# Optimization experiments

Hardware: AMD Instinct MI355X
Metric: run time of the kernel (lower is better)

Reference implementation:

```python
import jax, jax.numpy as jnp
import numpy as np

BETA = 0.45
GAMMA = 0.45
EPS = 1e-12  # F.normalize eps

N_PRED = 16384
N_GT = 32768


def setup_inputs() -> dict:
    key = jax.random.key(0)
    k1, k2, k3, k4 = jax.random.split(key, 4)
    pred_feat = jax.random.normal(k1, (N_PRED, 6), dtype=jnp.float32)
    gt_data = jax.random.normal(k2, (N_GT, 6), dtype=jnp.float32)
    R = jax.random.normal(k3, (3, 3), dtype=jnp.float32)
    t = jax.random.normal(k4, (3,), dtype=jnp.float32)
    s = jnp.ones((1,), dtype=jnp.float32)
    return {"pred_feat": pred_feat, "gt_data": gt_data, "R": R, "t": t, "s": s}


def _l2_normalize(x):
    # matches F.normalize(p=2, dim=1, eps=1e-12): x / max(||x||, eps)
    n = jnp.linalg.norm(x, axis=-1, keepdims=True)
    return x / jnp.maximum(n, EPS)


def reference(pred_feat, gt_data, R, t, s):
    # --- registration loss (R,t,s come from the external TEASER++ solver) ---
    I = jnp.eye(3, dtype=R.dtype)
    rot_loss = jnp.linalg.norm(R - I)          # Frobenius norm
    trans_loss = jnp.linalg.norm(t)            # L2 norm
    scale_loss = (s[0] - 1.0) ** 2
    reg_loss = rot_loss + trans_loss + scale_loss

    # --- nearest-neighbor normal loss ---
    pred_points = pred_feat[:, :3]   # [N,3]
    pred_normals = pred_feat[:, 3:]  # [N,3]
    gt_points = gt_data[:, :3]       # [L,3]
    gt_normals = gt_data[:, 3:]      # [L,3]

    # squared euclidean distances [N,L]; argmin identical to cdist argmin
    p2 = jnp.sum(pred_points * pred_points, axis=1, keepdims=True)  # [N,1]
    g2 = jnp.sum(gt_points * gt_points, axis=1)                     # [L]
    d2 = p2 + g2[None, :] - 2.0 * (pred_points @ gt_points.T)       # [N,L]
    min_indices = jnp.argmin(d2, axis=1)                            # [N]

    closest_gt_normals = gt_normals[min_indices]                    # [N,3]
    pred_u = _l2_normalize(pred_normals)
    gt_u = _l2_normalize(closest_gt_normals)
    cos_theta = jnp.sum(pred_u * gt_u, axis=1)
    norm_loss = jnp.mean(1.0 - cos_theta)

    return BETA * reg_loss + GAMMA * norm_loss
```

## Files before the change

kernel.cpp:

```cpp
#include <hip/hip_runtime.h>
#include <math.h>

#define NPRED 16384
#define NGT   32768
#define BETA  0.45f
#define GAMMA 0.45f

#define NGROUP 16
#define SPG    4
#define GSPLIT (NGROUP * SPG)
#define NTILE  (NGT / 32)
#define TPS    (NTILE / GSPLIT)
#define PB     256
#define NN_BX  (NPRED / PB)
#define RESB   (NPRED / 8)

typedef float f32x16 __attribute__((ext_vector_type(16)));
typedef short short8 __attribute__((ext_vector_type(8)));

__device__ __forceinline__ unsigned bf16h(float f) {
    unsigned u = __float_as_uint(f);
    return (u + 0x7FFFu + ((u >> 16) & 1u)) >> 16;
}
__device__ __forceinline__ float bf16f(unsigned h) { return __uint_as_float(h << 16); }
__device__ __forceinline__ unsigned pk2(unsigned lo, unsigned hi) { return lo | (hi << 16); }

#define MFMA_V(D, A, B, ZC)                                                    \
    asm("v_mfma_f32_32x32x16_bf16 %0, %1, %2, %3"                              \
        : "=&v"(D) : "v"(A), "v"(B), "v"(ZC))

__device__ __forceinline__ float tile_key(const f32x16 acc, int gtile) {
    const float m0 = fminf(fminf(acc[0],  acc[1]),  acc[2]);
    const float m1 = fminf(fminf(acc[3],  acc[4]),  acc[5]);
    const float m2 = fminf(fminf(acc[6],  acc[7]),  acc[8]);
    const float m3 = fminf(fminf(acc[9],  acc[10]), acc[11]);
    const float m4 = fminf(fminf(acc[12], acc[13]), acc[14]);
    const float n0 = fminf(fminf(m0, m1), m2);
    const float n1 = fminf(fminf(m3, m4), acc[15]);
    const float tmin = fminf(n0, n1);
    return __uint_as_float((__float_as_uint(tmin) & 0xFFFFFC00u) | (unsigned)gtile);
}

__global__ __launch_bounds__(256) void nn_kernel(
    const float* __restrict__ pred,
    const float* __restrict__ gt,
    unsigned* __restrict__ packed2)
{
    __shared__ uint4 AF[TPS * 64];

    const int l  = threadIdx.x & 63;
    const int w  = threadIdx.x >> 6;

    const int pbase = blockIdx.x * PB + w * 64;
    const int c     = l & 31;
    const bool hi   = l >= 32;
    uint4 bu0, bu1;
    {
        const int pi = pbase + c;
        const float x = pred[pi * 6 + 0], y = pred[pi * 6 + 1], zc = pred[pi * 6 + 2];
        const float mx = -2.0f * x, my = -2.0f * y, mz = -2.0f * zc;
        const unsigned xh = bf16h(mx), yh = bf16h(my), zh = bf16h(mz);
        const unsigned xl = bf16h(mx - bf16f(xh)), yl = bf16h(my - bf16f(yh));
        const unsigned zl = bf16h(mz - bf16f(zh));
        bu0.x = hi ? pk2(zh, zl) : pk2(xh, xl);
        bu0.y = bu0.x;
        bu0.z = hi ? 0x3F803F80u : pk2(yh, yl);
        bu0.w = hi ? 0u : bu0.z;
    }
    {
        const int pi = pbase + 32 + c;
        const float x = pred[pi * 6 + 0], y = pred[pi * 6 + 1], zc = pred[pi * 6 + 2];
        const float mx = -2.0f * x, my = -2.0f * y, mz = -2.0f * zc;
        const unsigned xh = bf16h(mx), yh = bf16h(my), zh = bf16h(mz);
        const unsigned xl = bf16h(mx - bf16f(xh)), yl = bf16h(my - bf16f(yh));
        const unsigned zl = bf16h(mz - bf16f(zh));
        bu1.x = hi ? pk2(zh, zl) : pk2(xh, xl);
        bu1.y = bu1.x;
        bu1.z = hi ? 0x3F803F80u : pk2(yh, yl);
        bu1.w = hi ? 0u : bu1.z;
    }
    const short8 bv0 = *(const short8*)&bu0;
    const short8 bv1 = *(const short8*)&bu1;
    const f32x16 zacc = {0.f,0.f,0.f,0.f,0.f,0.f,0.f,0.f,
                         0.f,0.f,0.f,0.f,0.f,0.f,0.f,0.f};

    float kmin0 = 1e30f, kmin1 = 1e30f;

#pragma unroll 1
    for (int u = 0; u < SPG; ++u) {
        const int sp = blockIdx.y * SPG + u;

        __syncthreads();
#pragma unroll
        for (int k = 0; k < 2; ++k) {
            const int lrow = threadIdx.x + k * 256;
            const int j = sp * (TPS * 32) + lrow;
            const float x = gt[j * 6 + 0], y = gt[j * 6 + 1], z = gt[j * 6 + 2];
            const float g2 = fmaf(x, x, fmaf(y, y, z * z));
            const unsigned xh = bf16h(x),  yh = bf16h(y),  zh = bf16h(z),  gh = bf16h(g2);
            const unsigned xl = bf16h(x - bf16f(xh)), yl = bf16h(y - bf16f(yh));
            const unsigned zl = bf16h(z - bf16f(zh)), gl = bf16h(g2 - bf16f(gh));
            const int tl = lrow >> 5, r = lrow & 31;
            AF[tl * 64 + r]      = make_uint4(pk2(xh, xh), pk2(xl, xl), pk2(yh, yh), pk2(yl, yl));
            AF[tl * 64 + 32 + r] = make_uint4(pk2(zh, zh), pk2(zl, zl), pk2(gh, gl), 0u);
        }
        __syncthreads();

        const int t0 = sp * TPS;
#pragma unroll 2
        for (int tt = 0; tt < TPS; tt += 2) {
            const uint4 aua = AF[tt * 64 + l];
            const uint4 aub = AF[(tt + 1) * 64 + l];
            const short8 ava = *(const short8*)&aua;
            const short8 avb = *(const short8*)&aub;
            const int ga = t0 + tt, gb = t0 + tt + 1;

            f32x16 acc_a0, acc_b0, acc_a1, acc_b1;
            MFMA_V(acc_a0, ava, bv0, zacc);
            MFMA_V(acc_b0, avb, bv0, zacc);
            MFMA_V(acc_a1, ava, bv1, zacc);
            MFMA_V(acc_b1, avb, bv1, zacc);

            kmin0 = fminf(kmin0, fminf(tile_key(acc_a0, ga), tile_key(acc_b0, gb)));
            kmin1 = fminf(kmin1, fminf(tile_key(acc_a1, ga), tile_key(acc_b1, gb)));
        }
    }

    kmin0 = fminf(kmin0, __shfl_xor(kmin0, 32, 64));
    kmin1 = fminf(kmin1, __shfl_xor(kmin1, 32, 64));

    const float km = hi ? kmin1 : kmin0;
    packed2[(size_t)(pbase + l) * NGROUP + blockIdx.y] = __float_as_uint(km);
}

__global__ __launch_bounds__(256) void rescan_kernel(
    const float* __restrict__ pred,
    const float* __restrict__ gt,
    const unsigned* __restrict__ packed2,
    float* __restrict__ partials)
{
    __shared__ float part[8];
    const int w = threadIdx.x >> 6, l = threadIdx.x & 63;
    const int half = l >> 5, jl = l & 31;
    const int pi = blockIdx.x * 8 + w * 2 + half;

    const unsigned* kp = packed2 + (size_t)pi * NGROUP;
    float e = (jl < NGROUP) ? __uint_as_float(kp[jl]) : 1e30f;
#pragma unroll
    for (int off = 16; off; off >>= 1)
        e = fminf(e, __shfl_xor(e, off, 32));
    const unsigned tix = __float_as_uint(e) & 0x3FFu;

    const int row = (int)tix * 32 + jl;
    const float2* gr = (const float2*)(gt + row * 6);
    const float2 ga = gr[0], gb = gr[1];
    const float gx = ga.x, gy = ga.y, gz = gb.x;
    const float g2 = fmaf(gx, gx, fmaf(gy, gy, gz * gz));
    const float2* pr = (const float2*)(pred + pi * 6);
    const float2 pa = pr[0], pb = pr[1];
    const float px = pa.x, py = pa.y, pz = pb.x;
    float d = fmaf(px, -2.0f * gx, fmaf(py, -2.0f * gy, fmaf(pz, -2.0f * gz, g2)));
    int jj = jl;
#pragma unroll
    for (int off = 16; off; off >>= 1) {
        const float d2 = __shfl_xor(d, off, 32);
        const int   j2 = __shfl_xor(jj, off, 32);
        const bool t = (d2 < d) || (d2 == d && j2 < jj);
        d  = t ? d2 : d;
        jj = t ? j2 : jj;
    }
    if (jl == 0) {
        const int idx = (int)tix * 32 + jj;
        const float nx = pred[pi * 6 + 3], ny = pred[pi * 6 + 4], nz = pred[pi * 6 + 5];
        const float ax = gt[idx * 6 + 3],  ay = gt[idx * 6 + 4],  az = gt[idx * 6 + 5];
        const float pn = fmaxf(sqrtf(fmaf(nx, nx, fmaf(ny, ny, nz * nz))), 1e-12f);
        const float gn = fmaxf(sqrtf(fmaf(ax, ax, fmaf(ay, ay, az * az))), 1e-12f);
        part[w * 2 + half] = 1.0f - fmaf(nx, ax, fmaf(ny, ay, nz * az)) / (pn * gn);
    }
    __syncthreads();
    if (threadIdx.x == 0) {
        float s = 0.f;
#pragma unroll
        for (int i = 0; i < 8; ++i) s += part[i];
        partials[blockIdx.x] = s;
    }
}

__global__ __launch_bounds__(256) void final_kernel(
    const float* __restrict__ partials,
    const float* __restrict__ Rm,
    const float* __restrict__ tv,
    const float* __restrict__ sv,
    float* __restrict__ out)
{
    __shared__ float ws_[4];
    float s = 0.f;
    for (int i = threadIdx.x; i < RESB; i += 256) s += partials[i];
#pragma unroll
    for (int off = 32; off; off >>= 1) s += __shfl_down(s, off, 64);
    if ((threadIdx.x & 63) == 0) ws_[threadIdx.x >> 6] = s;
    __syncthreads();
    if (threadIdx.x == 0) {
        const float t = ws_[0] + ws_[1] + ws_[2] + ws_[3];
        float rs = 0.f;
#pragma unroll
        for (int k = 0; k < 9; ++k) {
            const float v = Rm[k] - ((k % 4 == 0) ? 1.0f : 0.0f);
            rs = fmaf(v, v, rs);
        }
        const float rot = sqrtf(rs);
        const float tr  = sqrtf(fmaf(tv[0], tv[0], fmaf(tv[1], tv[1], tv[2] * tv[2])));
        const float sc  = (sv[0] - 1.0f) * (sv[0] - 1.0f);
        out[0] = GAMMA * t / (float)NPRED + BETA * (rot + tr + sc);
    }
}

extern "C" void kernel_launch(void* const* d_in, const int* in_sizes, int n_in,
                              void* d_out, int out_size, void* d_ws, size_t ws_size,
                              hipStream_t stream)
{
    const float* pred = (const float*)d_in[0];
    const float* gt   = (const float*)d_in[1];
    const float* Rm   = (const float*)d_in[2];
    const float* tv   = (const float*)d_in[3];
    const float* sv   = (const float*)d_in[4];
    float* out = (float*)d_out;

    unsigned* packed2 = (unsigned*)d_ws;
    float* partials   = (float*)((char*)d_ws + (size_t)NPRED * NGROUP * 4);

    nn_kernel<<<dim3(NN_BX, NGROUP), 256, 0, stream>>>(pred, gt, packed2);
    rescan_kernel<<<RESB, 256, 0, stream>>>(pred, gt, packed2, partials);
    final_kernel<<<1, 256, 0, stream>>>(partials, Rm, tv, sv, out);
}
```

Baseline: 34.81 us.

## Double-buffer GT tiles in LDS and hand-code min3 reductions via inline asm

Loads of the next GT chunk from global memory are issued before the MFMA loop over the current chunk, and are converted into a second LDS buffer afterwards. This hides global-load latency and cuts the barriers per chunk from two to one. The per-tile min reduction and key packing are rewritten with inline v_min3_f32 and v_and_or_b32, giving fewer VALU instructions per tile. The cost is double the LDS footprint and the loses of compiler scheduling freedom around the inline asm.

```diff
diff --git a/kernel.cpp b/kernel.cpp
--- a/kernel.cpp
+++ b/kernel.cpp
@@ -29,16 +29,29 @@
     asm("v_mfma_f32_32x32x16_bf16 %0, %1, %2, %3"                              \
         : "=&v"(D) : "v"(A), "v"(B), "v"(ZC))
 
-__device__ __forceinline__ float tile_key(const f32x16 acc, int gtile) {
-    const float m0 = fminf(fminf(acc[0],  acc[1]),  acc[2]);
-    const float m1 = fminf(fminf(acc[3],  acc[4]),  acc[5]);
-    const float m2 = fminf(fminf(acc[6],  acc[7]),  acc[8]);
-    const float m3 = fminf(fminf(acc[9],  acc[10]), acc[11]);
-    const float m4 = fminf(fminf(acc[12], acc[13]), acc[14]);
-    const float n0 = fminf(fminf(m0, m1), m2);
-    const float n1 = fminf(fminf(m3, m4), acc[15]);
-    const float tmin = fminf(n0, n1);
-    return __uint_as_float((__float_as_uint(tmin) & 0xFFFFFC00u) | (unsigned)gtile);
+__device__ __forceinline__ float tile_key3(const f32x16 acc, float vmask, int gtile) {
+    float m0, m1, m2, m3, m4, n0, n1, key;
+    asm("v_min3_f32 %0, %1, %2, %3" : "=v"(m0) : "v"(acc[0]),  "v"(acc[1]),  "v"(acc[2]));
+    asm("v_min3_f32 %0, %1, %2, %3" : "=v"(m1) : "v"(acc[3]),  "v"(acc[4]),  "v"(acc[5]));
+    asm("v_min3_f32 %0, %1, %2, %3" : "=v"(m2) : "v"(acc[6]),  "v"(acc[7]),  "v"(acc[8]));
+    asm("v_min3_f32 %0, %1, %2, %3" : "=v"(m3) : "v"(acc[9]),  "v"(acc[10]), "v"(acc[11]));
+    asm("v_min3_f32 %0, %1, %2, %3" : "=v"(m4) : "v"(acc[12]), "v"(acc[13]), "v"(acc[14]));
+    asm("v_min3_f32 %0, %1, %2, %3" : "=v"(n0) : "v"(m0), "v"(m1), "v"(m2));
+    asm("v_min3_f32 %0, %1, %2, %3" : "=v"(n1) : "v"(m3), "v"(m4), "v"(acc[15]));
+    asm("v_min_f32 %0, %1, %2"      : "=v"(key) : "v"(n0), "v"(n1));
+    asm("v_and_or_b32 %0, %1, %2, %3" : "+v"(key) : "v"(vmask), "s"(gtile));
+    return key;
+}
+
+__device__ __forceinline__ void conv_row(float x, float y, float z,
+                                         uint4* __restrict__ buf, int lrow) {
+    const float g2 = fmaf(x, x, fmaf(y, y, z * z));
+    const unsigned xh = bf16h(x),  yh = bf16h(y),  zh = bf16h(z),  gh = bf16h(g2);
+    const unsigned xl = bf16h(x - bf16f(xh)), yl = bf16h(y - bf16f(yh));
+    const unsigned zl = bf16h(z - bf16f(zh)), gl = bf16h(g2 - bf16f(gh));
+    const int tl = lrow >> 5, r = lrow & 31;
+    buf[tl * 64 + r]      = make_uint4(pk2(xh, xh), pk2(xl, xl), pk2(yh, yh), pk2(yl, yl));
+    buf[tl * 64 + 32 + r] = make_uint4(pk2(zh, zh), pk2(zl, zl), pk2(gh, gl), 0u);
 }
 
 __global__ __launch_bounds__(256) void nn_kernel(
@@ -46,7 +59,7 @@
     const float* __restrict__ gt,
     unsigned* __restrict__ packed2)
 {
-    __shared__ uint4 AF[TPS * 64];
+    __shared__ uint4 AF[2][TPS * 64];
 
     const int l  = threadIdx.x & 63;
     const int w  = threadIdx.x >> 6;
@@ -83,34 +96,43 @@
     const short8 bv1 = *(const short8*)&bu1;
     const f32x16 zacc = {0.f,0.f,0.f,0.f,0.f,0.f,0.f,0.f,
                          0.f,0.f,0.f,0.f,0.f,0.f,0.f,0.f};
+    const float vmask = __uint_as_float(0xFFFFFC00u);
 
     float kmin0 = 1e30f, kmin1 = 1e30f;
+    const int sp0 = blockIdx.y * SPG;
+
+    float2 r0a, r0b, r1a, r1b;
+    {
+        const int j0 = sp0 * 512 + threadIdx.x;
+        const float2* p0 = (const float2*)(gt + j0 * 6);
+        const float2* p1 = (const float2*)(gt + (j0 + 256) * 6);
+        r0a = p0[0]; r0b = p0[1];
+        r1a = p1[0]; r1b = p1[1];
+    }
+    conv_row(r0a.x, r0a.y, r0b.x, AF[0], threadIdx.x);
+    conv_row(r1a.x, r1a.y, r1b.x, AF[0], threadIdx.x + 256);
+    __syncthreads();
 
 #pragma unroll 1
     for (int u = 0; u < SPG; ++u) {
-        const int sp = blockIdx.y * SPG + u;
-
-        __syncthreads();
-#pragma unroll
-        for (int k = 0; k < 2; ++k) {
-            const int lrow = threadIdx.x + k * 256;
-            const int j = sp * (TPS * 32) + lrow;
-            const float x = gt[j * 6 + 0], y = gt[j * 6 + 1], z = gt[j * 6 + 2];
-            const float g2 = fmaf(x, x, fmaf(y, y, z * z));
-            const unsigned xh = bf16h(x),  yh = bf16h(y),  zh = bf16h(z),  gh = bf16h(g2);
-            const unsigned xl = bf16h(x - bf16f(xh)), yl = bf16h(y - bf16f(yh));
-            const unsigned zl = bf16h(z - bf16f(zh)), gl = bf16h(g2 - bf16f(gh));
-            const int tl = lrow >> 5, r = lrow & 31;
-            AF[tl * 64 + r]      = make_uint4(pk2(xh, xh), pk2(xl, xl), pk2(yh, yh), pk2(yl, yl));
-            AF[tl * 64 + 32 + r] = make_uint4(pk2(zh, zh), pk2(zl, zl), pk2(gh, gl), 0u);
-        }
-        __syncthreads();
+        const int sp = sp0 + u;
+        uint4* cur = AF[u & 1];
+        uint4* nxt = AF[(u + 1) & 1];
+        const bool more = (u + 1 < SPG);
+
+        if (more) {
+            const int j0 = (sp + 1) * 512 + threadIdx.x;
+            const float2* p0 = (const float2*)(gt + j0 * 6);
+            const float2* p1 = (const float2*)(gt + (j0 + 256) * 6);
+            r0a = p0[0]; r0b = p0[1];
+            r1a = p1[0]; r1b = p1[1];
+        }
 
         const int t0 = sp * TPS;
 #pragma unroll 2
         for (int tt = 0; tt < TPS; tt += 2) {
-            const uint4 aua = AF[tt * 64 + l];
-            const uint4 aub = AF[(tt + 1) * 64 + l];
+            const uint4 aua = cur[tt * 64 + l];
+            const uint4 aub = cur[(tt + 1) * 64 + l];
             const short8 ava = *(const short8*)&aua;
             const short8 avb = *(const short8*)&aub;
             const int ga = t0 + tt, gb = t0 + tt + 1;
@@ -121,9 +143,19 @@
             MFMA_V(acc_a1, ava, bv1, zacc);
             MFMA_V(acc_b1, avb, bv1, zacc);
 
-            kmin0 = fminf(kmin0, fminf(tile_key(acc_a0, ga), tile_key(acc_b0, gb)));
-            kmin1 = fminf(kmin1, fminf(tile_key(acc_a1, ga), tile_key(acc_b1, gb)));
-        }
+            const float ka0 = tile_key3(acc_a0, vmask, ga);
+            const float kb0 = tile_key3(acc_b0, vmask, gb);
+            asm("v_min3_f32 %0, %0, %1, %2" : "+v"(kmin0) : "v"(ka0), "v"(kb0));
+            const float ka1 = tile_key3(acc_a1, vmask, ga);
+            const float kb1 = tile_key3(acc_b1, vmask, gb);
+            asm("v_min3_f32 %0, %0, %1, %2" : "+v"(kmin1) : "v"(ka1), "v"(kb1));
+        }
+
+        if (more) {
+            conv_row(r0a.x, r0a.y, r0b.x, nxt, threadIdx.x);
+            conv_row(r1a.x, r1a.y, r1b.x, nxt, threadIdx.x + 256);
+        }
+        __syncthreads();
     }
 
     kmin0 = fminf(kmin0, __shfl_xor(kmin0, 32, 64));
```

Result: faster. 31.41 us (-9.8%).

## Split GT across 64 grid blocks, use min3 asm reductions and setprio

Applied to the files above, without the earlier changes.

Removes the per-block loop over four GT sub-tiles, so each block now stages one 512-point GT tile and the grid grows from 16 to 64 splits in y. This drops the repeated syncthreads and staging stalls and adds parallelism. The tile-min reduction is rewritten in inline asm using v_min3_f32 and v_and_or_b32 to cut VALU instruction count, and s_setprio is raised around the MFMA loop. The cost is four times more packed partial keys written and read by the rescan kernel.

```diff
diff --git a/kernel.cpp b/kernel.cpp
--- a/kernel.cpp
+++ b/kernel.cpp
@@ -6,9 +6,7 @@
 #define BETA  0.45f
 #define GAMMA 0.45f
 
-#define NGROUP 16
-#define SPG    4
-#define GSPLIT (NGROUP * SPG)
+#define GSPLIT 64
 #define NTILE  (NGT / 32)
 #define TPS    (NTILE / GSPLIT)
 #define PB     256
@@ -29,16 +27,18 @@
     asm("v_mfma_f32_32x32x16_bf16 %0, %1, %2, %3"                              \
         : "=&v"(D) : "v"(A), "v"(B), "v"(ZC))
 
-__device__ __forceinline__ float tile_key(const f32x16 acc, int gtile) {
-    const float m0 = fminf(fminf(acc[0],  acc[1]),  acc[2]);
-    const float m1 = fminf(fminf(acc[3],  acc[4]),  acc[5]);
-    const float m2 = fminf(fminf(acc[6],  acc[7]),  acc[8]);
-    const float m3 = fminf(fminf(acc[9],  acc[10]), acc[11]);
-    const float m4 = fminf(fminf(acc[12], acc[13]), acc[14]);
-    const float n0 = fminf(fminf(m0, m1), m2);
-    const float n1 = fminf(fminf(m3, m4), acc[15]);
-    const float tmin = fminf(n0, n1);
-    return __uint_as_float((__float_as_uint(tmin) & 0xFFFFFC00u) | (unsigned)gtile);
+__device__ __forceinline__ float tile_key3(const f32x16 acc, float vmask, int gtile) {
+    float m0, m1, m2, m3, m4, n0, n1, key;
+    asm("v_min3_f32 %0, %1, %2, %3" : "=v"(m0) : "v"(acc[0]),  "v"(acc[1]),  "v"(acc[2]));
+    asm("v_min3_f32 %0, %1, %2, %3" : "=v"(m1) : "v"(acc[3]),  "v"(acc[4]),  "v"(acc[5]));
+    asm("v_min3_f32 %0, %1, %2, %3" : "=v"(m2) : "v"(acc[6]),  "v"(acc[7]),  "v"(acc[8]));
+    asm("v_min3_f32 %0, %1, %2, %3" : "=v"(m3) : "v"(acc[9]),  "v"(acc[10]), "v"(acc[11]));
+    asm("v_min3_f32 %0, %1, %2, %3" : "=v"(m4) : "v"(acc[12]), "v"(acc[13]), "v"(acc[14]));
+    asm("v_min3_f32 %0, %1, %2, %3" : "=v"(n0) : "v"(m0), "v"(m1), "v"(m2));
+    asm("v_min3_f32 %0, %1, %2, %3" : "=v"(n1) : "v"(m3), "v"(m4), "v"(acc[15]));
+    asm("v_min_f32 %0, %1, %2"      : "=v"(key) : "v"(n0), "v"(n1));
+    asm("v_and_or_b32 %0, %1, %2, %3" : "+v"(key) : "v"(vmask), "s"(gtile));
+    return key;
 }
 
 __global__ __launch_bounds__(256) void nn_kernel(
@@ -50,6 +50,21 @@
 
     const int l  = threadIdx.x & 63;
     const int w  = threadIdx.x >> 6;
+    const int sp = blockIdx.y;
+
+#pragma unroll
+    for (int k = 0; k < 2; ++k) {
+        const int lrow = threadIdx.x + k * 256;
+        const int j = sp * 512 + lrow;
+        const float x = gt[j * 6 + 0], y = gt[j * 6 + 1], z = gt[j * 6 + 2];
+        const float g2 = fmaf(x, x, fmaf(y, y, z * z));
+        const unsigned xh = bf16h(x),  yh = bf16h(y),  zh = bf16h(z),  gh = bf16h(g2);
+        const unsigned xl = bf16h(x - bf16f(xh)), yl = bf16h(y - bf16f(yh));
+        const unsigned zl = bf16h(z - bf16f(zh)), gl = bf16h(g2 - bf16f(gh));
+        const int tl = lrow >> 5, r = lrow & 31;
+        AF[tl * 64 + r]      = make_uint4(pk2(xh, xh), pk2(xl, xl), pk2(yh, yh), pk2(yl, yl));
+        AF[tl * 64 + 32 + r] = make_uint4(pk2(zh, zh), pk2(zl, zl), pk2(gh, gl), 0u);
+    }
 
     const int pbase = blockIdx.x * PB + w * 64;
     const int c     = l & 31;
@@ -83,54 +98,41 @@
     const short8 bv1 = *(const short8*)&bu1;
     const f32x16 zacc = {0.f,0.f,0.f,0.f,0.f,0.f,0.f,0.f,
                          0.f,0.f,0.f,0.f,0.f,0.f,0.f,0.f};
+    const float vmask = __uint_as_float(0xFFFFFC00u);
 
     float kmin0 = 1e30f, kmin1 = 1e30f;
-
-#pragma unroll 1
-    for (int u = 0; u < SPG; ++u) {
-        const int sp = blockIdx.y * SPG + u;
-
-        __syncthreads();
-#pragma unroll
-        for (int k = 0; k < 2; ++k) {
-            const int lrow = threadIdx.x + k * 256;
-            const int j = sp * (TPS * 32) + lrow;
-            const float x = gt[j * 6 + 0], y = gt[j * 6 + 1], z = gt[j * 6 + 2];
-            const float g2 = fmaf(x, x, fmaf(y, y, z * z));
-            const unsigned xh = bf16h(x),  yh = bf16h(y),  zh = bf16h(z),  gh = bf16h(g2);
-            const unsigned xl = bf16h(x - bf16f(xh)), yl = bf16h(y - bf16f(yh));
-            const unsigned zl = bf16h(z - bf16f(zh)), gl = bf16h(g2 - bf16f(gh));
-            const int tl = lrow >> 5, r = lrow & 31;
-            AF[tl * 64 + r]      = make_uint4(pk2(xh, xh), pk2(xl, xl), pk2(yh, yh), pk2(yl, yl));
-            AF[tl * 64 + 32 + r] = make_uint4(pk2(zh, zh), pk2(zl, zl), pk2(gh, gl), 0u);
-        }
-        __syncthreads();
-
-        const int t0 = sp * TPS;
+    __syncthreads();
+
+    __builtin_amdgcn_s_setprio(1);
+    const int t0 = sp * TPS;
 #pragma unroll 2
-        for (int tt = 0; tt < TPS; tt += 2) {
-            const uint4 aua = AF[tt * 64 + l];
-            const uint4 aub = AF[(tt + 1) * 64 + l];
-            const short8 ava = *(const short8*)&aua;
-            const short8 avb = *(const short8*)&aub;
-            const int ga = t0 + tt, gb = t0 + tt + 1;
-
-            f32x16 acc_a0, acc_b0, acc_a1, acc_b1;
-            MFMA_V(acc_a0, ava, bv0, zacc);
-            MFMA_V(acc_b0, avb, bv0, zacc);
-            MFMA_V(acc_a1, ava, bv1, zacc);
-            MFMA_V(acc_b1, avb, bv1, zacc);
-
-            kmin0 = fminf(kmin0, fminf(tile_key(acc_a0, ga), tile_key(acc_b0, gb)));
-            kmin1 = fminf(kmin1, fminf(tile_key(acc_a1, ga), tile_key(acc_b1, gb)));
-        }
-    }
+    for (int tt = 0; tt < TPS; tt += 2) {
+        const uint4 aua = AF[tt * 64 + l];
+        const uint4 aub = AF[(tt + 1) * 64 + l];
+        const short8 ava = *(const short8*)&aua;
+        const short8 avb = *(const short8*)&aub;
+        const int ga = t0 + tt, gb = t0 + tt + 1;
+
+        f32x16 acc_a0, acc_b0, acc_a1, acc_b1;
+        MFMA_V(acc_a0, ava, bv0, zacc);
+        MFMA_V(acc_b0, avb, bv0, zacc);
+        MFMA_V(acc_a1, ava, bv1, zacc);
+        MFMA_V(acc_b1, avb, bv1, zacc);
+
+        const float ka0 = tile_key3(acc_a0, vmask, ga);
+        const float kb0 = tile_key3(acc_b0, vmask, gb);
+        asm("v_min3_f32 %0, %0, %1, %2" : "+v"(kmin0) : "v"(ka0), "v"(kb0));
+        const float ka1 = tile_key3(acc_a1, vmask, ga);
+        const float kb1 = tile_key3(acc_b1, vmask, gb);
+        asm("v_min3_f32 %0, %0, %1, %2" : "+v"(kmin1) : "v"(ka1), "v"(kb1));
+    }
+    __builtin_amdgcn_s_setprio(0);
 
     kmin0 = fminf(kmin0, __shfl_xor(kmin0, 32, 64));
     kmin1 = fminf(kmin1, __shfl_xor(kmin1, 32, 64));
 
     const float km = hi ? kmin1 : kmin0;
-    packed2[(size_t)(pbase + l) * NGROUP + blockIdx.y] = __float_as_uint(km);
+    packed2[(size_t)(pbase + l) * GSPLIT + sp] = __float_as_uint(km);
 }
 
 __global__ __launch_bounds__(256) void rescan_kernel(
@@ -144,8 +146,8 @@
     const int half = l >> 5, jl = l & 31;
     const int pi = blockIdx.x * 8 + w * 2 + half;
 
-    const unsigned* kp = packed2 + (size_t)pi * NGROUP;
-    float e = (jl < NGROUP) ? __uint_as_float(kp[jl]) : 1e30f;
+    const unsigned* kp = packed2 + (size_t)pi * GSPLIT;
+    float e = fminf(__uint_as_float(kp[jl]), __uint_as_float(kp[jl + 32]));
 #pragma unroll
     for (int off = 16; off; off >>= 1)
         e = fminf(e, __shfl_xor(e, off, 32));
@@ -227,9 +229,9 @@
     float* out = (float*)d_out;
 
     unsigned* packed2 = (unsigned*)d_ws;
-    float* partials   = (float*)((char*)d_ws + (size_t)NPRED * NGROUP * 4);
-
-    nn_kernel<<<dim3(NN_BX, NGROUP), 256, 0, stream>>>(pred, gt, packed2);
+    float* partials   = (float*)((char*)d_ws + (size_t)NPRED * GSPLIT * 4);
+
+    nn_kernel<<<dim3(NN_BX, GSPLIT), 256, 0, stream>>>(pred, gt, packed2);
     rescan_kernel<<<RESB, 256, 0, stream>>>(pred, gt, packed2, partials);
     final_kernel<<<1, 256, 0, stream>>>(partials, Rm, tv, sv, out);
 }
```

Result: no change. 34.18 us (-1.8%).
